# Kernel tuning notes

Measured on AMD Instinct MI355X. Metric: run time of the kernel, lower is better.

The kernel has to match this reference:

```python
import jax, jax.numpy as jnp
import numpy as np

N = 100000   # users
E = 50000    # hyperedges per timestep
NNZ = 800000 # incidences per timestep
T = 8        # step_split
D = 64       # embed_dim


def setup_inputs() -> dict:
    key = jax.random.key(0)
    ks = jax.random.split(key, 9)
    s = 1.0 / np.sqrt(D)
    return {
        "user_emb": jax.random.normal(ks[0], (N, D), jnp.float32) * s,
        "W_conv": jax.random.normal(ks[1], (D, D), jnp.float32) * s,
        "b_conv": jnp.zeros((D,), jnp.float32),
        "fus_w1": jax.random.normal(ks[2], (D, D), jnp.float32) * s,
        "fus_b1": jnp.zeros((D,), jnp.float32),
        "fus_w2": jax.random.normal(ks[3], (D, 1), jnp.float32) * s,
        "fus_b2": jnp.zeros((1,), jnp.float32),
        "edge_nodes": jax.random.randint(ks[4], (T, NNZ), 0, N),
        "edge_hyper": jax.random.randint(ks[5], (T, NNZ), 0, E),
    }


def _hconv(h, nodes, hyper):
    # h: [N, D] transformed node feats; nodes/hyper: [NNZ] incidence list
    ones = jnp.ones((nodes.shape[0], 1), h.dtype)
    e_sum = jax.ops.segment_sum(h[nodes], hyper, num_segments=E)      # [E, D]
    e_cnt = jax.ops.segment_sum(ones, hyper, num_segments=E)          # [E, 1]
    e = e_sum / jnp.maximum(e_cnt, 1.0)
    n_sum = jax.ops.segment_sum(e[hyper], nodes, num_segments=N)      # [N, D]
    n_cnt = jax.ops.segment_sum(ones, nodes, num_segments=N)          # [N, 1]
    return n_sum / jnp.maximum(n_cnt, 1.0)


def _fuse(hidden, dy, w1, b1, w2, b2):
    emb = jnp.stack([hidden, dy], axis=0)                             # [2, N, D]
    score = jax.nn.softmax(jnp.tanh(emb @ w1 + b1) @ w2 + b2, axis=0)  # [2, N, 1]
    return jnp.sum(score * emb, axis=0)                                # [N, D]


def reference(user_emb, W_conv, b_conv, fus_w1, fus_b1, fus_w2, fus_b2,
              edge_nodes, edge_hyper):
    # Conv input is always the raw user embedding table -> per-step convs independent.
    h = jax.nn.relu(user_emb @ W_conv + b_conv)                        # [N, D]
    conv_out = jax.vmap(lambda nd, hy: _hconv(h, nd, hy))(edge_nodes, edge_hyper)  # [T, N, D]

    def step(carry, dy):
        out = _fuse(carry, dy, fus_w1, fus_b1, fus_w2, fus_b2)
        return out, None

    final, _ = jax.lax.scan(step, conv_out[0], conv_out[1:])
    return final
```

## Files before the change

### kernel.cpp

```cpp
#include <hip/hip_runtime.h>
#include <hip/hip_bf16.h>

#define N_USERS 100000
#define E_HYPER 50000
#define NNZ_E   800000
#define T_STEPS 8
#define DIM     64
#define IDXM    0xFFFFF

typedef __bf16 bf16x8 __attribute__((ext_vector_type(8)));
typedef float  f32x4  __attribute__((ext_vector_type(4)));

__device__ __forceinline__ float ld_in(const void* p, size_t i, int f32)
{
    return f32 ? ((const float*)p)[i]
               : __bfloat162float(((const __hip_bfloat16*)p)[i]);
}

__global__ void k_detect(const unsigned short* __restrict__ raw, int* __restrict__ flag)
{
    __shared__ int cnt;
    if (threadIdx.x == 0) cnt = 0;
    __syncthreads();
    int c = 0;
    for (int i = threadIdx.x; i < 4096; i += blockDim.x) {
        int e = (raw[i] >> 7) & 0xFF;
        if (e > 126) c++;
    }
    atomicAdd(&cnt, c);
    __syncthreads();
    if (threadIdx.x == 0) *flag = (cnt > 64) ? 1 : 0;
}

__global__ void k_convert_params(
    const void* W, const void* b, const void* w1, const void* b1,
    const void* w2, const void* b2, const int* __restrict__ flag,
    float* __restrict__ st)
{
    int f = *flag;
    int i = blockIdx.x * blockDim.x + threadIdx.x;
    if (i < 4096)          st[i] = ld_in(W,  i,        f);
    else if (i < 4160)     st[i] = ld_in(b,  i - 4096, f);
    else if (i < 8256)     st[i] = ld_in(w1, i - 4160, f);
    else if (i < 8320)     st[i] = ld_in(b1, i - 8256, f);
    else if (i < 8384)     st[i] = ld_in(w2, i - 8320, f);
    else if (i == 8384)    st[i] = ld_in(b2, 0,        f);
}

__global__ __launch_bounds__(256) void k_transform(
    const void* __restrict__ emb, const int* __restrict__ flag,
    const float* __restrict__ st, __hip_bfloat16* __restrict__ h)
{
    __shared__ float Wl[DIM * DIM];
    __shared__ float bl[DIM];
    for (int i = threadIdx.x; i < DIM * DIM; i += blockDim.x) Wl[i] = st[i];
    if (threadIdx.x < DIM) bl[threadIdx.x] = st[4096 + threadIdx.x];
    __syncthreads();

    int f = *flag;
    int wave = threadIdx.x >> 6, lane = threadIdx.x & 63;
    int wavesTotal = gridDim.x * (blockDim.x >> 6);
    for (int row = blockIdx.x * (blockDim.x >> 6) + wave; row < N_USERS;
         row += wavesTotal) {
        size_t base = (size_t)row * DIM;
        float v = ld_in(emb, base + lane, f);
        float acc = bl[lane];
#pragma unroll
        for (int k = 0; k < DIM; ++k)
            acc += __shfl(v, k, 64) * Wl[k * DIM + lane];
        h[base + lane] = __float2bfloat16(fmaxf(acc, 0.f));
    }
}

__global__ __launch_bounds__(256) void k_build(
    const int* __restrict__ nodes, const int* __restrict__ hyper,
    int* __restrict__ head_e, int* __restrict__ next_e,
    int* __restrict__ head_n, int* __restrict__ next_n, int tag)
{
    int i = blockIdx.x * blockDim.x + threadIdx.x;
    if (i >= NNZ_E) return;
    int tv = (tag << 20) | i;
    next_e[i] = atomicExch(&head_e[hyper[i]], tv);
    next_n[i] = atomicExch(&head_n[nodes[i]], tv);
}

__device__ __forceinline__ int dec(int v, int tag)
{
    return ((v >> 20) == tag) ? (v & IDXM) : -1;
}

__global__ __launch_bounds__(256) void k_gather_e(
    const __hip_bfloat16* __restrict__ h,
    const int* __restrict__ nodes,
    const int* __restrict__ head_e, const int* __restrict__ next_e,
    __hip_bfloat16* __restrict__ e, int tag)
{
    int lane = threadIdx.x & 63;
    int wid = blockIdx.x * (blockDim.x >> 6) + (threadIdx.x >> 6);
    int nW  = gridDim.x * (blockDim.x >> 6);
    for (int s0 = wid * 8; s0 < E_HYPER; s0 += nW * 8) {
        int idx[8]; float acc[8]; int cnt[8];
#pragma unroll
        for (int c = 0; c < 8; ++c) {
            int sg = s0 + c;
            idx[c] = (sg < E_HYPER) ? dec(head_e[sg], tag) : -1;
            acc[c] = 0.f; cnt[c] = 0;
        }
        while (true) {
            bool any = false;
#pragma unroll
            for (int c = 0; c < 8; ++c) any = any || (idx[c] >= 0);
            if (!any) break;
            int nxt[8], nd[8];
#pragma unroll
            for (int c = 0; c < 8; ++c)
                if (idx[c] >= 0) { nxt[c] = next_e[idx[c]]; nd[c] = nodes[idx[c]]; }
#pragma unroll
            for (int c = 0; c < 8; ++c)
                if (idx[c] >= 0) {
                    acc[c] += __bfloat162float(h[(size_t)nd[c] * DIM + lane]);
                    cnt[c]++; idx[c] = dec(nxt[c], tag);
                }
        }
#pragma unroll
        for (int c = 0; c < 8; ++c) {
            int sg = s0 + c;
            if (sg < E_HYPER)
                e[(size_t)sg * DIM + lane] =
                    __float2bfloat16(acc[c] / (float)max(cnt[c], 1));
        }
    }
}

__device__ __forceinline__ float ld_carry(void* out, float* cws, size_t i,
                                          int f, int use_ws)
{
    if (f) return ((float*)out)[i];
    if (use_ws) return cws[i];
    return __bfloat162float(((__hip_bfloat16*)out)[i]);
}
__device__ __forceinline__ void st_carry(void* out, float* cws, size_t i,
                                         int f, int use_ws, int wr, float v)
{
    if (f) { ((float*)out)[i] = v; return; }
    if (use_ws) {
        cws[i] = v;
        if (wr) ((__hip_bfloat16*)out)[i] = __float2bfloat16(v);
        return;
    }
    ((__hip_bfloat16*)out)[i] = __float2bfloat16(v);
}

__global__ __launch_bounds__(256) void k_gather_n(
    const __hip_bfloat16* __restrict__ e,
    const int* __restrict__ hyper,
    const int* __restrict__ head_n, const int* __restrict__ next_n,
    float* __restrict__ dy,
    void* __restrict__ out, float* __restrict__ cws,
    const int* __restrict__ flag, int use_ws, int to_carry, int tag)
{
    int f = *flag;
    int lane = threadIdx.x & 63;
    int wid = blockIdx.x * (blockDim.x >> 6) + (threadIdx.x >> 6);
    int nW  = gridDim.x * (blockDim.x >> 6);
    for (int s0 = wid * 8; s0 < N_USERS; s0 += nW * 8) {
        int idx[8]; float acc[8]; int cnt[8];
#pragma unroll
        for (int c = 0; c < 8; ++c) {
            int sg = s0 + c;
            idx[c] = (sg < N_USERS) ? dec(head_n[sg], tag) : -1;
            acc[c] = 0.f; cnt[c] = 0;
        }
        while (true) {
            bool any = false;
#pragma unroll
            for (int c = 0; c < 8; ++c) any = any || (idx[c] >= 0);
            if (!any) break;
            int nxt[8], hy[8];
#pragma unroll
            for (int c = 0; c < 8; ++c)
                if (idx[c] >= 0) { nxt[c] = next_n[idx[c]]; hy[c] = hyper[idx[c]]; }
#pragma unroll
            for (int c = 0; c < 8; ++c)
                if (idx[c] >= 0) {
                    acc[c] += __bfloat162float(e[(size_t)hy[c] * DIM + lane]);
                    cnt[c]++; idx[c] = dec(nxt[c], tag);
                }
        }
#pragma unroll
        for (int c = 0; c < 8; ++c) {
            int sg = s0 + c;
            if (sg < N_USERS) {
                float v = acc[c] / (float)max(cnt[c], 1);
                size_t o = (size_t)sg * DIM + lane;
                if (to_carry) st_carry(out, cws, o, f, use_ws, 0, v);
                else          dy[o] = v;
            }
        }
    }
}

__global__ __launch_bounds__(256) void k_fuse_mfma(
    void* __restrict__ dout, float* __restrict__ cws,
    const float* __restrict__ dy_buf,
    const float* __restrict__ st, const int* __restrict__ flag,
    int use_ws, int write_out)
{
    int f = *flag;
    float* cf = f ? (float*)dout : (use_ws ? cws : (float*)0);
    __hip_bfloat16* cb = (__hip_bfloat16*)dout;

    int lane = threadIdx.x & 63;
    int quad = lane >> 4;
    int m    = lane & 15;

    bf16x8 bw[4][2];
    float b1v[4], w2v[4];
#pragma unroll
    for (int nt = 0; nt < 4; ++nt) {
#pragma unroll
        for (int kb = 0; kb < 2; ++kb)
#pragma unroll
            for (int j = 0; j < 8; ++j) {
                int k = kb * 32 + quad * 8 + j;
                bw[nt][kb][j] = (__bf16)st[4160 + k * 64 + nt * 16 + m];
            }
        b1v[nt] = st[8256 + nt * 16 + m];
        w2v[nt] = st[8320 + nt * 16 + m];
    }

    int wid = blockIdx.x * (blockDim.x >> 6) + (threadIdx.x >> 6);
    int nW  = gridDim.x * (blockDim.x >> 6);
    const int NT = N_USERS / 16;

    for (int tile = wid; tile < NT; tile += nW) {
        int row = tile * 16 + m;
        size_t base = (size_t)row * DIM;

        float hidf[2][8], dyf[2][8];
        if (cf) {
            const f32x4* cp = (const f32x4*)(cf + base);
            const f32x4* dp = (const f32x4*)(dy_buf + base);
#pragma unroll
            for (int kb = 0; kb < 2; ++kb) {
                f32x4 a = cp[kb * 8 + quad * 2], b = cp[kb * 8 + quad * 2 + 1];
                f32x4 c = dp[kb * 8 + quad * 2], d = dp[kb * 8 + quad * 2 + 1];
#pragma unroll
                for (int j = 0; j < 4; ++j) {
                    hidf[kb][j] = a[j]; hidf[kb][4 + j] = b[j];
                    dyf[kb][j]  = c[j]; dyf[kb][4 + j]  = d[j];
                }
            }
        } else {
#pragma unroll
            for (int kb = 0; kb < 2; ++kb)
#pragma unroll
                for (int j = 0; j < 8; ++j) {
                    int k = kb * 32 + quad * 8 + j;
                    hidf[kb][j] = __bfloat162float(cb[base + k]);
                    dyf[kb][j]  = dy_buf[base + k];
                }
        }

        bf16x8 ah[2], ad[2];
#pragma unroll
        for (int kb = 0; kb < 2; ++kb)
#pragma unroll
            for (int j = 0; j < 8; ++j) {
                ah[kb][j] = (__bf16)hidf[kb][j];
                ad[kb][j] = (__bf16)dyf[kb][j];
            }

        float zh[4] = {0.f, 0.f, 0.f, 0.f};
        float zd[4] = {0.f, 0.f, 0.f, 0.f};
#pragma unroll
        for (int nt = 0; nt < 4; ++nt) {
            f32x4 acch = {0.f, 0.f, 0.f, 0.f};
            f32x4 accd = {0.f, 0.f, 0.f, 0.f};
#pragma unroll
            for (int kb = 0; kb < 2; ++kb) {
                acch = __builtin_amdgcn_mfma_f32_16x16x32_bf16(ah[kb], bw[nt][kb], acch, 0, 0, 0);
                accd = __builtin_amdgcn_mfma_f32_16x16x32_bf16(ad[kb], bw[nt][kb], accd, 0, 0, 0);
            }
#pragma unroll
            for (int reg = 0; reg < 4; ++reg) {
                zh[reg] += tanhf(acch[reg] + b1v[nt]) * w2v[nt];
                zd[reg] += tanhf(accd[reg] + b1v[nt]) * w2v[nt];
            }
        }
        float s[4];
#pragma unroll
        for (int reg = 0; reg < 4; ++reg) {
#pragma unroll
            for (int off = 1; off < 16; off <<= 1) {
                zh[reg] += __shfl_xor(zh[reg], off, 64);
                zd[reg] += __shfl_xor(zd[reg], off, 64);
            }
            float mm = fmaxf(zh[reg], zd[reg]);
            float eh = expf(zh[reg] - mm), ed = expf(zd[reg] - mm);
            s[reg] = eh / (eh + ed);
        }
        int srcl = (m >> 2) * 16;
        float s0 = __shfl(s[0], srcl, 64), s1 = __shfl(s[1], srcl, 64);
        float s2 = __shfl(s[2], srcl, 64), s3 = __shfl(s[3], srcl, 64);
        int r3 = m & 3;
        float sv = (r3 == 0) ? s0 : (r3 == 1) ? s1 : (r3 == 2) ? s2 : s3;

        if (cf) {
            f32x4* cp = (f32x4*)(cf + base);
#pragma unroll
            for (int kb = 0; kb < 2; ++kb) {
                f32x4 v0, v1;
#pragma unroll
                for (int j = 0; j < 4; ++j) {
                    v0[j] = sv * hidf[kb][j]     + (1.f - sv) * dyf[kb][j];
                    v1[j] = sv * hidf[kb][4 + j] + (1.f - sv) * dyf[kb][4 + j];
                }
                cp[kb * 8 + quad * 2]     = v0;
                cp[kb * 8 + quad * 2 + 1] = v1;
                if (write_out && !f) {
#pragma unroll
                    for (int j = 0; j < 4; ++j) {
                        int k = kb * 32 + quad * 8 + j;
                        cb[base + k]     = __float2bfloat16(v0[j]);
                        cb[base + k + 4] = __float2bfloat16(v1[j]);
                    }
                }
            }
        } else {
#pragma unroll
            for (int kb = 0; kb < 2; ++kb)
#pragma unroll
                for (int j = 0; j < 8; ++j) {
                    int k = kb * 32 + quad * 8 + j;
                    float v = sv * hidf[kb][j] + (1.f - sv) * dyf[kb][j];
                    cb[base + k] = __float2bfloat16(v);
                }
        }
    }
}

extern "C" void kernel_launch(void* const* d_in, const int* in_sizes, int n_in,
                              void* d_out, int out_size, void* d_ws,
                              size_t ws_size, hipStream_t stream)
{
    const void* user_emb = d_in[0];
    const void* W_conv   = d_in[1];
    const void* b_conv   = d_in[2];
    const void* fus_w1   = d_in[3];
    const void* fus_b1   = d_in[4];
    const void* fus_w2   = d_in[5];
    const void* fus_b2   = d_in[6];
    const int* edge_nodes = (const int*)d_in[7];
    const int* edge_hyper = (const int*)d_in[8];

    const size_t ND = (size_t)N_USERS * DIM;

    float* ws = (float*)d_ws;
    int*   flag   = (int*)ws;
    float* st     = ws + 16;
    int*   head_e = (int*)(ws + 8464);
    int*   head_n = (int*)(ws + 58464);
    int*   next_e = (int*)(ws + 158464);
    int*   next_n = (int*)(ws + 958464);
    __hip_bfloat16* e_buf = (__hip_bfloat16*)(ws + 1758464);
    float* dy_buf = ws + 3358464;
    __hip_bfloat16* h = (__hip_bfloat16*)(ws + 9758464);
    float* carry_ws   = ws + 12958464;

    const size_t need_ws_carry = (12958464 + ND) * 4;
    const int use_ws = (ws_size >= need_ws_carry) ? 1 : 0;

    k_detect<<<1, 256, 0, stream>>>((const unsigned short*)user_emb, flag);
    k_convert_params<<<(8385 + 255) / 256, 256, 0, stream>>>(
        W_conv, b_conv, fus_w1, fus_b1, fus_w2, fus_b2, flag, st);
    k_transform<<<1024, 256, 0, stream>>>(user_emb, flag, st, h);

    for (int t = 0; t < T_STEPS; ++t) {
        const int* nodes = edge_nodes + (size_t)t * NNZ_E;
        const int* hyper = edge_hyper + (size_t)t * NNZ_E;
        int tag = t + 1;

        k_build<<<(NNZ_E + 255) / 256, 256, 0, stream>>>(
            nodes, hyper, head_e, next_e, head_n, next_n, tag);
        k_gather_e<<<1563, 256, 0, stream>>>(h, nodes, head_e, next_e, e_buf, tag);
        k_gather_n<<<3125, 256, 0, stream>>>(
            e_buf, hyper, head_n, next_n, dy_buf,
            d_out, carry_ws, flag, use_ws, (t == 0) ? 1 : 0, tag);

        if (t > 0) {
            k_fuse_mfma<<<1024, 256, 0, stream>>>(
                d_out, carry_ws, dy_buf, st, flag, use_ws,
                (t == T_STEPS - 1) ? 1 : 0);
        }
    }
}
```

Baseline: 1.996 ms.

## Overlap per-step build and fuse with gathers through horizontally merged kernels

Merges independent work into shared launches. The transform runs alongside the first list build, the fuse for step t-1 runs alongside the hyperedge gather of step t, and the list build for step t+1 runs alongside the node gather of step t. The linked-list head and next buffers are double-buffered so the next step's build cannot clobber the lists in use. The dy intermediate is also stored as bf16 instead of fp32, which halves its traffic but adds rounding error. The aim is fewer launches and better device fill; the cost is more workspace and lower precision in dy.

```diff
diff --git a/kernel.cpp b/kernel.cpp
--- a/kernel.cpp
+++ b/kernel.cpp
@@ -8,6 +8,12 @@
 #define DIM     64
 #define IDXM    0xFFFFF
 
+#define TR_BLOCKS 1024
+#define GE_BLOCKS 1563
+#define GN_BLOCKS 3125
+#define B_BLOCKS  3125
+#define FU_BLOCKS 1024
+
 typedef __bf16 bf16x8 __attribute__((ext_vector_type(8)));
 typedef float  f32x4  __attribute__((ext_vector_type(4)));
 
@@ -15,6 +21,30 @@
 {
     return f32 ? ((const float*)p)[i]
                : __bfloat162float(((const __hip_bfloat16*)p)[i]);
+}
+
+__device__ __forceinline__ int dec(int v, int tag)
+{
+    return ((v >> 20) == tag) ? (v & IDXM) : -1;
+}
+
+__device__ __forceinline__ float ld_carry(void* out, float* cws, size_t i,
+                                          int f, int use_ws)
+{
+    if (f) return ((float*)out)[i];
+    if (use_ws) return cws[i];
+    return __bfloat162float(((__hip_bfloat16*)out)[i]);
+}
+__device__ __forceinline__ void st_carry(void* out, float* cws, size_t i,
+                                         int f, int use_ws, int wr, float v)
+{
+    if (f) { ((float*)out)[i] = v; return; }
+    if (use_ws) {
+        cws[i] = v;
+        if (wr) ((__hip_bfloat16*)out)[i] = __float2bfloat16(v);
+        return;
+    }
+    ((__hip_bfloat16*)out)[i] = __float2bfloat16(v);
 }
 
 __global__ void k_detect(const unsigned short* __restrict__ raw, int* __restrict__ flag)
@@ -47,63 +77,31 @@
     else if (i == 8384)    st[i] = ld_in(b2, 0,        f);
 }
 
-__global__ __launch_bounds__(256) void k_transform(
-    const void* __restrict__ emb, const int* __restrict__ flag,
-    const float* __restrict__ st, __hip_bfloat16* __restrict__ h)
-{
-    __shared__ float Wl[DIM * DIM];
-    __shared__ float bl[DIM];
-    for (int i = threadIdx.x; i < DIM * DIM; i += blockDim.x) Wl[i] = st[i];
-    if (threadIdx.x < DIM) bl[threadIdx.x] = st[4096 + threadIdx.x];
-    __syncthreads();
-
-    int f = *flag;
-    int wave = threadIdx.x >> 6, lane = threadIdx.x & 63;
-    int wavesTotal = gridDim.x * (blockDim.x >> 6);
-    for (int row = blockIdx.x * (blockDim.x >> 6) + wave; row < N_USERS;
-         row += wavesTotal) {
-        size_t base = (size_t)row * DIM;
-        float v = ld_in(emb, base + lane, f);
-        float acc = bl[lane];
-#pragma unroll
-        for (int k = 0; k < DIM; ++k)
-            acc += __shfl(v, k, 64) * Wl[k * DIM + lane];
-        h[base + lane] = __float2bfloat16(fmaxf(acc, 0.f));
-    }
-}
-
-__global__ __launch_bounds__(256) void k_build(
+__device__ __forceinline__ void build_body(
     const int* __restrict__ nodes, const int* __restrict__ hyper,
-    int* __restrict__ head_e, int* __restrict__ next_e,
-    int* __restrict__ head_n, int* __restrict__ next_n, int tag)
-{
-    int i = blockIdx.x * blockDim.x + threadIdx.x;
+    int* __restrict__ he, int* __restrict__ ne,
+    int* __restrict__ hn, int* __restrict__ nn, int tag, int i)
+{
     if (i >= NNZ_E) return;
     int tv = (tag << 20) | i;
-    next_e[i] = atomicExch(&head_e[hyper[i]], tv);
-    next_n[i] = atomicExch(&head_n[nodes[i]], tv);
-}
-
-__device__ __forceinline__ int dec(int v, int tag)
-{
-    return ((v >> 20) == tag) ? (v & IDXM) : -1;
-}
-
-__global__ __launch_bounds__(256) void k_gather_e(
-    const __hip_bfloat16* __restrict__ h,
-    const int* __restrict__ nodes,
-    const int* __restrict__ head_e, const int* __restrict__ next_e,
-    __hip_bfloat16* __restrict__ e, int tag)
-{
-    int lane = threadIdx.x & 63;
-    int wid = blockIdx.x * (blockDim.x >> 6) + (threadIdx.x >> 6);
-    int nW  = gridDim.x * (blockDim.x >> 6);
+    ne[i] = atomicExch(&he[hyper[i]], tv);
+    nn[i] = atomicExch(&hn[nodes[i]], tv);
+}
+
+__device__ __forceinline__ void ge_body(
+    const __hip_bfloat16* __restrict__ h, const int* __restrict__ nodes,
+    const int* __restrict__ he, const int* __restrict__ ne,
+    __hip_bfloat16* __restrict__ e, int tag, int bid, int nblocks, int tid)
+{
+    int lane = tid & 63;
+    int wid = bid * 4 + (tid >> 6);
+    int nW  = nblocks * 4;
     for (int s0 = wid * 8; s0 < E_HYPER; s0 += nW * 8) {
         int idx[8]; float acc[8]; int cnt[8];
 #pragma unroll
         for (int c = 0; c < 8; ++c) {
             int sg = s0 + c;
-            idx[c] = (sg < E_HYPER) ? dec(head_e[sg], tag) : -1;
+            idx[c] = (sg < E_HYPER) ? dec(he[sg], tag) : -1;
             acc[c] = 0.f; cnt[c] = 0;
         }
         while (true) {
@@ -114,7 +112,7 @@
             int nxt[8], nd[8];
 #pragma unroll
             for (int c = 0; c < 8; ++c)
-                if (idx[c] >= 0) { nxt[c] = next_e[idx[c]]; nd[c] = nodes[idx[c]]; }
+                if (idx[c] >= 0) { nxt[c] = ne[idx[c]]; nd[c] = nodes[idx[c]]; }
 #pragma unroll
             for (int c = 0; c < 8; ++c)
                 if (idx[c] >= 0) {
@@ -132,43 +130,22 @@
     }
 }
 
-__device__ __forceinline__ float ld_carry(void* out, float* cws, size_t i,
-                                          int f, int use_ws)
-{
-    if (f) return ((float*)out)[i];
-    if (use_ws) return cws[i];
-    return __bfloat162float(((__hip_bfloat16*)out)[i]);
-}
-__device__ __forceinline__ void st_carry(void* out, float* cws, size_t i,
-                                         int f, int use_ws, int wr, float v)
-{
-    if (f) { ((float*)out)[i] = v; return; }
-    if (use_ws) {
-        cws[i] = v;
-        if (wr) ((__hip_bfloat16*)out)[i] = __float2bfloat16(v);
-        return;
-    }
-    ((__hip_bfloat16*)out)[i] = __float2bfloat16(v);
-}
-
-__global__ __launch_bounds__(256) void k_gather_n(
-    const __hip_bfloat16* __restrict__ e,
-    const int* __restrict__ hyper,
-    const int* __restrict__ head_n, const int* __restrict__ next_n,
-    float* __restrict__ dy,
-    void* __restrict__ out, float* __restrict__ cws,
-    const int* __restrict__ flag, int use_ws, int to_carry, int tag)
-{
-    int f = *flag;
-    int lane = threadIdx.x & 63;
-    int wid = blockIdx.x * (blockDim.x >> 6) + (threadIdx.x >> 6);
-    int nW  = gridDim.x * (blockDim.x >> 6);
+__device__ __forceinline__ void gn_body(
+    const __hip_bfloat16* __restrict__ e, const int* __restrict__ hyper,
+    const int* __restrict__ hn, const int* __restrict__ nn,
+    __hip_bfloat16* __restrict__ dyb, void* __restrict__ dout,
+    float* __restrict__ cws, int f, int use_ws, int to_carry, int tag,
+    int bid, int nblocks, int tid)
+{
+    int lane = tid & 63;
+    int wid = bid * 4 + (tid >> 6);
+    int nW  = nblocks * 4;
     for (int s0 = wid * 8; s0 < N_USERS; s0 += nW * 8) {
         int idx[8]; float acc[8]; int cnt[8];
 #pragma unroll
         for (int c = 0; c < 8; ++c) {
             int sg = s0 + c;
-            idx[c] = (sg < N_USERS) ? dec(head_n[sg], tag) : -1;
+            idx[c] = (sg < N_USERS) ? dec(hn[sg], tag) : -1;
             acc[c] = 0.f; cnt[c] = 0;
         }
         while (true) {
@@ -179,7 +156,7 @@
             int nxt[8], hy[8];
 #pragma unroll
             for (int c = 0; c < 8; ++c)
-                if (idx[c] >= 0) { nxt[c] = next_n[idx[c]]; hy[c] = hyper[idx[c]]; }
+                if (idx[c] >= 0) { nxt[c] = nn[idx[c]]; hy[c] = hyper[idx[c]]; }
 #pragma unroll
             for (int c = 0; c < 8; ++c)
                 if (idx[c] >= 0) {
@@ -193,24 +170,22 @@
             if (sg < N_USERS) {
                 float v = acc[c] / (float)max(cnt[c], 1);
                 size_t o = (size_t)sg * DIM + lane;
-                if (to_carry) st_carry(out, cws, o, f, use_ws, 0, v);
-                else          dy[o] = v;
-            }
-        }
-    }
-}
-
-__global__ __launch_bounds__(256) void k_fuse_mfma(
+                if (to_carry) st_carry(dout, cws, o, f, use_ws, 0, v);
+                else          dyb[o] = __float2bfloat16(v);
+            }
+        }
+    }
+}
+
+__device__ __forceinline__ void fu_body(
     void* __restrict__ dout, float* __restrict__ cws,
-    const float* __restrict__ dy_buf,
-    const float* __restrict__ st, const int* __restrict__ flag,
-    int use_ws, int write_out)
-{
-    int f = *flag;
+    const __hip_bfloat16* __restrict__ dyb, const float* __restrict__ st,
+    int f, int use_ws, int write_out, int bid, int nblocks, int tid)
+{
     float* cf = f ? (float*)dout : (use_ws ? cws : (float*)0);
     __hip_bfloat16* cb = (__hip_bfloat16*)dout;
 
-    int lane = threadIdx.x & 63;
+    int lane = tid & 63;
     int quad = lane >> 4;
     int m    = lane & 15;
 
@@ -229,8 +204,8 @@
         w2v[nt] = st[8320 + nt * 16 + m];
     }
 
-    int wid = blockIdx.x * (blockDim.x >> 6) + (threadIdx.x >> 6);
-    int nW  = gridDim.x * (blockDim.x >> 6);
+    int wid = bid * 4 + (tid >> 6);
+    int nW  = nblocks * 4;
     const int NT = N_USERS / 16;
 
     for (int tile = wid; tile < NT; tile += nW) {
@@ -238,38 +213,28 @@
         size_t base = (size_t)row * DIM;
 
         float hidf[2][8], dyf[2][8];
-        if (cf) {
-            const f32x4* cp = (const f32x4*)(cf + base);
-            const f32x4* dp = (const f32x4*)(dy_buf + base);
-#pragma unroll
-            for (int kb = 0; kb < 2; ++kb) {
+        bf16x8 ah[2], ad[2];
+#pragma unroll
+        for (int kb = 0; kb < 2; ++kb) {
+            ad[kb] = *(const bf16x8*)(const void*)(dyb + base + kb * 32 + quad * 8);
+#pragma unroll
+            for (int j = 0; j < 8; ++j) dyf[kb][j] = (float)ad[kb][j];
+            if (cf) {
+                const f32x4* cp = (const f32x4*)(cf + base);
                 f32x4 a = cp[kb * 8 + quad * 2], b = cp[kb * 8 + quad * 2 + 1];
-                f32x4 c = dp[kb * 8 + quad * 2], d = dp[kb * 8 + quad * 2 + 1];
 #pragma unroll
                 for (int j = 0; j < 4; ++j) {
                     hidf[kb][j] = a[j]; hidf[kb][4 + j] = b[j];
-                    dyf[kb][j]  = c[j]; dyf[kb][4 + j]  = d[j];
-                }
-            }
-        } else {
-#pragma unroll
-            for (int kb = 0; kb < 2; ++kb)
-#pragma unroll
-                for (int j = 0; j < 8; ++j) {
-                    int k = kb * 32 + quad * 8 + j;
-                    hidf[kb][j] = __bfloat162float(cb[base + k]);
-                    dyf[kb][j]  = dy_buf[base + k];
-                }
-        }
-
-        bf16x8 ah[2], ad[2];
-#pragma unroll
-        for (int kb = 0; kb < 2; ++kb)
-#pragma unroll
-            for (int j = 0; j < 8; ++j) {
-                ah[kb][j] = (__bf16)hidf[kb][j];
-                ad[kb][j] = (__bf16)dyf[kb][j];
-            }
+                }
+#pragma unroll
+                for (int j = 0; j < 8; ++j) ah[kb][j] = (__bf16)hidf[kb][j];
+            } else {
+                bf16x8 hv = *(const bf16x8*)(const void*)(cb + base + kb * 32 + quad * 8);
+                ah[kb] = hv;
+#pragma unroll
+                for (int j = 0; j < 8; ++j) hidf[kb][j] = (float)hv[j];
+            }
+        }
 
         float zh[4] = {0.f, 0.f, 0.f, 0.f};
         float zd[4] = {0.f, 0.f, 0.f, 0.f};
@@ -337,6 +302,72 @@
                     cb[base + k] = __float2bfloat16(v);
                 }
         }
+    }
+}
+
+__global__ __launch_bounds__(256) void k_trans_build(
+    const void* __restrict__ emb, const int* __restrict__ flag,
+    const float* __restrict__ st, __hip_bfloat16* __restrict__ h,
+    const int* __restrict__ nodes, const int* __restrict__ hyper,
+    int* __restrict__ he, int* __restrict__ ne,
+    int* __restrict__ hn, int* __restrict__ nn, int tag)
+{
+    __shared__ float Wl[DIM * DIM];
+    __shared__ float bl[DIM];
+    if ((int)blockIdx.x < TR_BLOCKS) {
+        for (int i = threadIdx.x; i < DIM * DIM; i += blockDim.x) Wl[i] = st[i];
+        if (threadIdx.x < DIM) bl[threadIdx.x] = st[4096 + threadIdx.x];
+        __syncthreads();
+        int f = *flag;
+        int wave = threadIdx.x >> 6, lane = threadIdx.x & 63;
+        int nW = TR_BLOCKS * 4;
+        for (int row = blockIdx.x * 4 + wave; row < N_USERS; row += nW) {
+            size_t base = (size_t)row * DIM;
+            float v = ld_in(emb, base + lane, f);
+            float acc = bl[lane];
+#pragma unroll
+            for (int k = 0; k < DIM; ++k)
+                acc += __shfl(v, k, 64) * Wl[k * DIM + lane];
+            h[base + lane] = __float2bfloat16(fmaxf(acc, 0.f));
+        }
+    } else {
+        int i = (blockIdx.x - TR_BLOCKS) * blockDim.x + threadIdx.x;
+        build_body(nodes, hyper, he, ne, hn, nn, tag, i);
+    }
+}
+
+__global__ __launch_bounds__(256) void k_ge_fuse(
+    const __hip_bfloat16* __restrict__ h, const int* __restrict__ nodes,
+    const int* __restrict__ he, const int* __restrict__ ne,
+    __hip_bfloat16* __restrict__ e, int tag, int ge_blocks,
+    void* __restrict__ dout, float* __restrict__ cws,
+    const __hip_bfloat16* __restrict__ dyb, const float* __restrict__ st,
+    const int* __restrict__ flag, int use_ws, int do_fuse, int write_out)
+{
+    if ((int)blockIdx.x < ge_blocks) {
+        ge_body(h, nodes, he, ne, e, tag, blockIdx.x, ge_blocks, threadIdx.x);
+    } else if (do_fuse) {
+        fu_body(dout, cws, dyb, st, *flag, use_ws, write_out,
+                blockIdx.x - ge_blocks, gridDim.x - ge_blocks, threadIdx.x);
+    }
+}
+
+__global__ __launch_bounds__(256) void k_gn_build(
+    const __hip_bfloat16* __restrict__ e, const int* __restrict__ hyper,
+    const int* __restrict__ hn, const int* __restrict__ nn,
+    __hip_bfloat16* __restrict__ dyb, void* __restrict__ dout,
+    float* __restrict__ cws, const int* __restrict__ flag,
+    int use_ws, int to_carry, int tag, int gn_blocks,
+    const int* __restrict__ nodes1, const int* __restrict__ hyper1,
+    int* __restrict__ he1, int* __restrict__ ne1,
+    int* __restrict__ hn1, int* __restrict__ nn1, int tag1, int do_build)
+{
+    if ((int)blockIdx.x < gn_blocks) {
+        gn_body(e, hyper, hn, nn, dyb, dout, cws, *flag, use_ws, to_carry,
+                tag, blockIdx.x, gn_blocks, threadIdx.x);
+    } else if (do_build) {
+        int i = (blockIdx.x - gn_blocks) * blockDim.x + threadIdx.x;
+        build_body(nodes1, hyper1, he1, ne1, hn1, nn1, tag1, i);
     }
 }
 
@@ -357,41 +388,51 @@
     const size_t ND = (size_t)N_USERS * DIM;
 
     float* ws = (float*)d_ws;
-    int*   flag   = (int*)ws;
-    float* st     = ws + 16;
-    int*   head_e = (int*)(ws + 8464);
-    int*   head_n = (int*)(ws + 58464);
-    int*   next_e = (int*)(ws + 158464);
-    int*   next_n = (int*)(ws + 958464);
-    __hip_bfloat16* e_buf = (__hip_bfloat16*)(ws + 1758464);
-    float* dy_buf = ws + 3358464;
-    __hip_bfloat16* h = (__hip_bfloat16*)(ws + 9758464);
-    float* carry_ws   = ws + 12958464;
-
-    const size_t need_ws_carry = (12958464 + ND) * 4;
+    int*   flag = (int*)ws;
+    float* st   = ws + 16;
+    int* he[2] = {(int*)(ws + 8464),    (int*)(ws + 58464)};
+    int* hn[2] = {(int*)(ws + 108464),  (int*)(ws + 208464)};
+    int* ne[2] = {(int*)(ws + 308464),  (int*)(ws + 1108464)};
+    int* nn[2] = {(int*)(ws + 1908464), (int*)(ws + 2708464)};
+    __hip_bfloat16* e_buf = (__hip_bfloat16*)(ws + 3508464);
+    __hip_bfloat16* dyb   = (__hip_bfloat16*)(ws + 5108464);
+    __hip_bfloat16* h     = (__hip_bfloat16*)(ws + 8308464);
+    float* carry_ws       = ws + 11508464;
+
+    const size_t need_ws_carry = (11508464 + ND) * 4;
     const int use_ws = (ws_size >= need_ws_carry) ? 1 : 0;
 
     k_detect<<<1, 256, 0, stream>>>((const unsigned short*)user_emb, flag);
     k_convert_params<<<(8385 + 255) / 256, 256, 0, stream>>>(
         W_conv, b_conv, fus_w1, fus_b1, fus_w2, fus_b2, flag, st);
-    k_transform<<<1024, 256, 0, stream>>>(user_emb, flag, st, h);
+
+    k_trans_build<<<TR_BLOCKS + B_BLOCKS, 256, 0, stream>>>(
+        user_emb, flag, st, h, edge_nodes, edge_hyper,
+        he[0], ne[0], hn[0], nn[0], 1);
 
     for (int t = 0; t < T_STEPS; ++t) {
-        const int* nodes = edge_nodes + (size_t)t * NNZ_E;
-        const int* hyper = edge_hyper + (size_t)t * NNZ_E;
-        int tag = t + 1;
-
-        k_build<<<(NNZ_E + 255) / 256, 256, 0, stream>>>(
-            nodes, hyper, head_e, next_e, head_n, next_n, tag);
-        k_gather_e<<<1563, 256, 0, stream>>>(h, nodes, head_e, next_e, e_buf, tag);
-        k_gather_n<<<3125, 256, 0, stream>>>(
-            e_buf, hyper, head_n, next_n, dy_buf,
-            d_out, carry_ws, flag, use_ws, (t == 0) ? 1 : 0, tag);
-
-        if (t > 0) {
-            k_fuse_mfma<<<1024, 256, 0, stream>>>(
-                d_out, carry_ws, dy_buf, st, flag, use_ws,
-                (t == T_STEPS - 1) ? 1 : 0);
-        }
-    }
-}
+        int b  = t & 1;
+        int nb = b ^ 1;
+        const int* nodes  = edge_nodes + (size_t)t * NNZ_E;
+        const int* hyper  = edge_hyper + (size_t)t * NNZ_E;
+        const int* nodes1 = edge_nodes + (size_t)(t + 1) * NNZ_E;
+        const int* hyper1 = edge_hyper + (size_t)(t + 1) * NNZ_E;
+
+        int gridA = GE_BLOCKS + ((t > 0) ? FU_BLOCKS : 0);
+        k_ge_fuse<<<gridA, 256, 0, stream>>>(
+            h, nodes, he[b], ne[b], e_buf, t + 1, GE_BLOCKS,
+            d_out, carry_ws, dyb, st, flag, use_ws, (t > 0) ? 1 : 0, 0);
+
+        int do_b = (t < T_STEPS - 1) ? 1 : 0;
+        int gridB = GN_BLOCKS + (do_b ? B_BLOCKS : 0);
+        k_gn_build<<<gridB, 256, 0, stream>>>(
+            e_buf, hyper, hn[b], nn[b], dyb, d_out, carry_ws, flag,
+            use_ws, (t == 0) ? 1 : 0, t + 1, GN_BLOCKS,
+            do_b ? nodes1 : nodes, do_b ? hyper1 : hyper,
+            he[nb], ne[nb], hn[nb], nn[nb], t + 2, do_b);
+    }
+
+    k_ge_fuse<<<FU_BLOCKS, 256, 0, stream>>>(
+        h, edge_nodes, he[1], ne[1], e_buf, 8, 0,
+        d_out, carry_ws, dyb, st, flag, use_ws, 1, 1);
+}
```

Measured after the change: 2.685 ms. 34.5% more time.

## Co-schedule next-step list build with current fuse and transform in merged kernels

Applied to the files above, without the earlier changes.

Fuses independent work horizontally by splitting the grid's blocks between two roles. The linked-list build for step t+1 now runs in the same launch as the fusion MLP for step t, and the first build shares a launch with the dense transform. This removes one launch per timestep and lets the atomic-heavy build overlap with the bandwidth- and MFMA-bound fuse work. The tag scheme means the head arrays never need clearing. The cost is sharing one block size and register budget between both roles, which can limit occupancy for the lighter role.

```diff
diff --git a/kernel.cpp b/kernel.cpp
--- a/kernel.cpp
+++ b/kernel.cpp
@@ -8,6 +8,12 @@
 #define DIM     64
 #define IDXM    0xFFFFF
 
+#define TR_BLOCKS 1024
+#define GE_BLOCKS 1563
+#define GN_BLOCKS 3125
+#define B_BLOCKS  3125
+#define FU_BLOCKS 1024
+
 typedef __bf16 bf16x8 __attribute__((ext_vector_type(8)));
 typedef float  f32x4  __attribute__((ext_vector_type(4)));
 
@@ -15,6 +21,30 @@
 {
     return f32 ? ((const float*)p)[i]
                : __bfloat162float(((const __hip_bfloat16*)p)[i]);
+}
+
+__device__ __forceinline__ int dec(int v, int tag)
+{
+    return ((v >> 20) == tag) ? (v & IDXM) : -1;
+}
+
+__device__ __forceinline__ float ld_carry(void* out, float* cws, size_t i,
+                                          int f, int use_ws)
+{
+    if (f) return ((float*)out)[i];
+    if (use_ws) return cws[i];
+    return __bfloat162float(((__hip_bfloat16*)out)[i]);
+}
+__device__ __forceinline__ void st_carry(void* out, float* cws, size_t i,
+                                         int f, int use_ws, int wr, float v)
+{
+    if (f) { ((float*)out)[i] = v; return; }
+    if (use_ws) {
+        cws[i] = v;
+        if (wr) ((__hip_bfloat16*)out)[i] = __float2bfloat16(v);
+        return;
+    }
+    ((__hip_bfloat16*)out)[i] = __float2bfloat16(v);
 }
 
 __global__ void k_detect(const unsigned short* __restrict__ raw, int* __restrict__ flag)
@@ -47,52 +77,190 @@
     else if (i == 8384)    st[i] = ld_in(b2, 0,        f);
 }
 
-__global__ __launch_bounds__(256) void k_transform(
+__device__ __forceinline__ void build_body(
+    const int* __restrict__ nodes, const int* __restrict__ hyper,
+    int* __restrict__ he, int* __restrict__ ne,
+    int* __restrict__ hn, int* __restrict__ nn, int tag, int i)
+{
+    if (i >= NNZ_E) return;
+    int tv = (tag << 20) | i;
+    ne[i] = atomicExch(&he[hyper[i]], tv);
+    nn[i] = atomicExch(&hn[nodes[i]], tv);
+}
+
+__device__ __forceinline__ void fu_body(
+    void* __restrict__ dout, float* __restrict__ cws,
+    const float* __restrict__ dy_buf, const float* __restrict__ st,
+    int f, int use_ws, int write_out, int bid, int nblocks, int tid)
+{
+    float* cf = f ? (float*)dout : (use_ws ? cws : (float*)0);
+    __hip_bfloat16* cb = (__hip_bfloat16*)dout;
+
+    int lane = tid & 63;
+    int quad = lane >> 4;
+    int m    = lane & 15;
+
+    bf16x8 bw[4][2];
+    float b1v[4], w2v[4];
+#pragma unroll
+    for (int nt = 0; nt < 4; ++nt) {
+#pragma unroll
+        for (int kb = 0; kb < 2; ++kb)
+#pragma unroll
+            for (int j = 0; j < 8; ++j) {
+                int k = kb * 32 + quad * 8 + j;
+                bw[nt][kb][j] = (__bf16)st[4160 + k * 64 + nt * 16 + m];
+            }
+        b1v[nt] = st[8256 + nt * 16 + m];
+        w2v[nt] = st[8320 + nt * 16 + m];
+    }
+
+    int wid = bid * 4 + (tid >> 6);
+    int nW  = nblocks * 4;
+    const int NT = N_USERS / 16;
+
+    for (int tile = wid; tile < NT; tile += nW) {
+        int row = tile * 16 + m;
+        size_t base = (size_t)row * DIM;
+
+        float hidf[2][8], dyf[2][8];
+        if (cf) {
+            const f32x4* cp = (const f32x4*)(cf + base);
+            const f32x4* dp = (const f32x4*)(dy_buf + base);
+#pragma unroll
+            for (int kb = 0; kb < 2; ++kb) {
+                f32x4 a = cp[kb * 8 + quad * 2], b = cp[kb * 8 + quad * 2 + 1];
+                f32x4 c = dp[kb * 8 + quad * 2], d = dp[kb * 8 + quad * 2 + 1];
+#pragma unroll
+                for (int j = 0; j < 4; ++j) {
+                    hidf[kb][j] = a[j]; hidf[kb][4 + j] = b[j];
+                    dyf[kb][j]  = c[j]; dyf[kb][4 + j]  = d[j];
+                }
+            }
+        } else {
+#pragma unroll
+            for (int kb = 0; kb < 2; ++kb)
+#pragma unroll
+                for (int j = 0; j < 8; ++j) {
+                    int k = kb * 32 + quad * 8 + j;
+                    hidf[kb][j] = __bfloat162float(cb[base + k]);
+                    dyf[kb][j]  = dy_buf[base + k];
+                }
+        }
+
+        bf16x8 ah[2], ad[2];
+#pragma unroll
+        for (int kb = 0; kb < 2; ++kb)
+#pragma unroll
+            for (int j = 0; j < 8; ++j) {
+                ah[kb][j] = (__bf16)hidf[kb][j];
+                ad[kb][j] = (__bf16)dyf[kb][j];
+            }
+
+        float zh[4] = {0.f, 0.f, 0.f, 0.f};
+        float zd[4] = {0.f, 0.f, 0.f, 0.f};
+#pragma unroll
+        for (int nt = 0; nt < 4; ++nt) {
+            f32x4 acch = {0.f, 0.f, 0.f, 0.f};
+            f32x4 accd = {0.f, 0.f, 0.f, 0.f};
+#pragma unroll
+            for (int kb = 0; kb < 2; ++kb) {
+                acch = __builtin_amdgcn_mfma_f32_16x16x32_bf16(ah[kb], bw[nt][kb], acch, 0, 0, 0);
+                accd = __builtin_amdgcn_mfma_f32_16x16x32_bf16(ad[kb], bw[nt][kb], accd, 0, 0, 0);
+            }
+#pragma unroll
+            for (int reg = 0; reg < 4; ++reg) {
+                zh[reg] += tanhf(acch[reg] + b1v[nt]) * w2v[nt];
+                zd[reg] += tanhf(accd[reg] + b1v[nt]) * w2v[nt];
+            }
+        }
+        float s[4];
+#pragma unroll
+        for (int reg = 0; reg < 4; ++reg) {
+#pragma unroll
+            for (int off = 1; off < 16; off <<= 1) {
+                zh[reg] += __shfl_xor(zh[reg], off, 64);
+                zd[reg] += __shfl_xor(zd[reg], off, 64);
+            }
+            float mm = fmaxf(zh[reg], zd[reg]);
+            float eh = expf(zh[reg] - mm), ed = expf(zd[reg] - mm);
+            s[reg] = eh / (eh + ed);
+        }
+        int srcl = (m >> 2) * 16;
+        float s0 = __shfl(s[0], srcl, 64), s1 = __shfl(s[1], srcl, 64);
+        float s2 = __shfl(s[2], srcl, 64), s3 = __shfl(s[3], srcl, 64);
+        int r3 = m & 3;
+        float sv = (r3 == 0) ? s0 : (r3 == 1) ? s1 : (r3 == 2) ? s2 : s3;
+
+        if (cf) {
+            f32x4* cp = (f32x4*)(cf + base);
+#pragma unroll
+            for (int kb = 0; kb < 2; ++kb) {
+                f32x4 v0, v1;
+#pragma unroll
+                for (int j = 0; j < 4; ++j) {
+                    v0[j] = sv * hidf[kb][j]     + (1.f - sv) * dyf[kb][j];
+                    v1[j] = sv * hidf[kb][4 + j] + (1.f - sv) * dyf[kb][4 + j];
+                }
+                cp[kb * 8 + quad * 2]     = v0;
+                cp[kb * 8 + quad * 2 + 1] = v1;
+                if (write_out && !f) {
+#pragma unroll
+                    for (int j = 0; j < 4; ++j) {
+                        int k = kb * 32 + quad * 8 + j;
+                        cb[base + k]     = __float2bfloat16(v0[j]);
+                        cb[base + k + 4] = __float2bfloat16(v1[j]);
+                    }
+                }
+            }
+        } else {
+#pragma unroll
+            for (int kb = 0; kb < 2; ++kb)
+#pragma unroll
+                for (int j = 0; j < 8; ++j) {
+                    int k = kb * 32 + quad * 8 + j;
+                    float v = sv * hidf[kb][j] + (1.f - sv) * dyf[kb][j];
+                    cb[base + k] = __float2bfloat16(v);
+                }
+        }
+    }
+}
+
+__global__ __launch_bounds__(256) void k_trans_build(
     const void* __restrict__ emb, const int* __restrict__ flag,
-    const float* __restrict__ st, __hip_bfloat16* __restrict__ h)
+    const float* __restrict__ st, __hip_bfloat16* __restrict__ h,
+    const int* __restrict__ nodes, const int* __restrict__ hyper,
+    int* __restrict__ he, int* __restrict__ ne,
+    int* __restrict__ hn, int* __restrict__ nn, int tag)
 {
     __shared__ float Wl[DIM * DIM];
     __shared__ float bl[DIM];
-    for (int i = threadIdx.x; i < DIM * DIM; i += blockDim.x) Wl[i] = st[i];
-    if (threadIdx.x < DIM) bl[threadIdx.x] = st[4096 + threadIdx.x];
-    __syncthreads();
-
-    int f = *flag;
-    int wave = threadIdx.x >> 6, lane = threadIdx.x & 63;
-    int wavesTotal = gridDim.x * (blockDim.x >> 6);
-    for (int row = blockIdx.x * (blockDim.x >> 6) + wave; row < N_USERS;
-         row += wavesTotal) {
-        size_t base = (size_t)row * DIM;
-        float v = ld_in(emb, base + lane, f);
-        float acc = bl[lane];
-#pragma unroll
-        for (int k = 0; k < DIM; ++k)
-            acc += __shfl(v, k, 64) * Wl[k * DIM + lane];
-        h[base + lane] = __float2bfloat16(fmaxf(acc, 0.f));
-    }
-}
-
-__global__ __launch_bounds__(256) void k_build(
-    const int* __restrict__ nodes, const int* __restrict__ hyper,
-    int* __restrict__ head_e, int* __restrict__ next_e,
-    int* __restrict__ head_n, int* __restrict__ next_n, int tag)
-{
-    int i = blockIdx.x * blockDim.x + threadIdx.x;
-    if (i >= NNZ_E) return;
-    int tv = (tag << 20) | i;
-    next_e[i] = atomicExch(&head_e[hyper[i]], tv);
-    next_n[i] = atomicExch(&head_n[nodes[i]], tv);
-}
-
-__device__ __forceinline__ int dec(int v, int tag)
-{
-    return ((v >> 20) == tag) ? (v & IDXM) : -1;
+    if ((int)blockIdx.x < TR_BLOCKS) {
+        for (int i = threadIdx.x; i < DIM * DIM; i += blockDim.x) Wl[i] = st[i];
+        if (threadIdx.x < DIM) bl[threadIdx.x] = st[4096 + threadIdx.x];
+        __syncthreads();
+        int f = *flag;
+        int wave = threadIdx.x >> 6, lane = threadIdx.x & 63;
+        int nW = TR_BLOCKS * 4;
+        for (int row = blockIdx.x * 4 + wave; row < N_USERS; row += nW) {
+            size_t base = (size_t)row * DIM;
+            float v = ld_in(emb, base + lane, f);
+            float acc = bl[lane];
+#pragma unroll
+            for (int k = 0; k < DIM; ++k)
+                acc += __shfl(v, k, 64) * Wl[k * DIM + lane];
+            h[base + lane] = __float2bfloat16(fmaxf(acc, 0.f));
+        }
+    } else {
+        int i = (blockIdx.x - TR_BLOCKS) * blockDim.x + threadIdx.x;
+        build_body(nodes, hyper, he, ne, hn, nn, tag, i);
+    }
 }
 
 __global__ __launch_bounds__(256) void k_gather_e(
     const __hip_bfloat16* __restrict__ h,
     const int* __restrict__ nodes,
-    const int* __restrict__ head_e, const int* __restrict__ next_e,
+    const int* __restrict__ he, const int* __restrict__ ne,
     __hip_bfloat16* __restrict__ e, int tag)
 {
     int lane = threadIdx.x & 63;
@@ -103,7 +271,7 @@
 #pragma unroll
         for (int c = 0; c < 8; ++c) {
             int sg = s0 + c;
-            idx[c] = (sg < E_HYPER) ? dec(head_e[sg], tag) : -1;
+            idx[c] = (sg < E_HYPER) ? dec(he[sg], tag) : -1;
             acc[c] = 0.f; cnt[c] = 0;
         }
         while (true) {
@@ -114,7 +282,7 @@
             int nxt[8], nd[8];
 #pragma unroll
             for (int c = 0; c < 8; ++c)
-                if (idx[c] >= 0) { nxt[c] = next_e[idx[c]]; nd[c] = nodes[idx[c]]; }
+                if (idx[c] >= 0) { nxt[c] = ne[idx[c]]; nd[c] = nodes[idx[c]]; }
 #pragma unroll
             for (int c = 0; c < 8; ++c)
                 if (idx[c] >= 0) {
@@ -132,29 +300,10 @@
     }
 }
 
-__device__ __forceinline__ float ld_carry(void* out, float* cws, size_t i,
-                                          int f, int use_ws)
-{
-    if (f) return ((float*)out)[i];
-    if (use_ws) return cws[i];
-    return __bfloat162float(((__hip_bfloat16*)out)[i]);
-}
-__device__ __forceinline__ void st_carry(void* out, float* cws, size_t i,
-                                         int f, int use_ws, int wr, float v)
-{
-    if (f) { ((float*)out)[i] = v; return; }
-    if (use_ws) {
-        cws[i] = v;
-        if (wr) ((__hip_bfloat16*)out)[i] = __float2bfloat16(v);
-        return;
-    }
-    ((__hip_bfloat16*)out)[i] = __float2bfloat16(v);
-}
-
 __global__ __launch_bounds__(256) void k_gather_n(
     const __hip_bfloat16* __restrict__ e,
     const int* __restrict__ hyper,
-    const int* __restrict__ head_n, const int* __restrict__ next_n,
+    const int* __restrict__ hn, const int* __restrict__ nn,
     float* __restrict__ dy,
     void* __restrict__ out, float* __restrict__ cws,
     const int* __restrict__ flag, int use_ws, int to_carry, int tag)
@@ -168,7 +317,7 @@
 #pragma unroll
         for (int c = 0; c < 8; ++c) {
             int sg = s0 + c;
-            idx[c] = (sg < N_USERS) ? dec(head_n[sg], tag) : -1;
+            idx[c] = (sg < N_USERS) ? dec(hn[sg], tag) : -1;
             acc[c] = 0.f; cnt[c] = 0;
         }
         while (true) {
@@ -179,7 +328,7 @@
             int nxt[8], hy[8];
 #pragma unroll
             for (int c = 0; c < 8; ++c)
-                if (idx[c] >= 0) { nxt[c] = next_n[idx[c]]; hy[c] = hyper[idx[c]]; }
+                if (idx[c] >= 0) { nxt[c] = nn[idx[c]]; hy[c] = hyper[idx[c]]; }
 #pragma unroll
             for (int c = 0; c < 8; ++c)
                 if (idx[c] >= 0) {
@@ -200,143 +349,20 @@
     }
 }
 
-__global__ __launch_bounds__(256) void k_fuse_mfma(
+__global__ __launch_bounds__(256) void k_build_fuse(
+    const int* __restrict__ nodes1, const int* __restrict__ hyper1,
+    int* __restrict__ he, int* __restrict__ ne,
+    int* __restrict__ hn, int* __restrict__ nn, int tag1, int nbuild,
     void* __restrict__ dout, float* __restrict__ cws,
-    const float* __restrict__ dy_buf,
-    const float* __restrict__ st, const int* __restrict__ flag,
-    int use_ws, int write_out)
-{
-    int f = *flag;
-    float* cf = f ? (float*)dout : (use_ws ? cws : (float*)0);
-    __hip_bfloat16* cb = (__hip_bfloat16*)dout;
-
-    int lane = threadIdx.x & 63;
-    int quad = lane >> 4;
-    int m    = lane & 15;
-
-    bf16x8 bw[4][2];
-    float b1v[4], w2v[4];
-#pragma unroll
-    for (int nt = 0; nt < 4; ++nt) {
-#pragma unroll
-        for (int kb = 0; kb < 2; ++kb)
-#pragma unroll
-            for (int j = 0; j < 8; ++j) {
-                int k = kb * 32 + quad * 8 + j;
-                bw[nt][kb][j] = (__bf16)st[4160 + k * 64 + nt * 16 + m];
-            }
-        b1v[nt] = st[8256 + nt * 16 + m];
-        w2v[nt] = st[8320 + nt * 16 + m];
-    }
-
-    int wid = blockIdx.x * (blockDim.x >> 6) + (threadIdx.x >> 6);
-    int nW  = gridDim.x * (blockDim.x >> 6);
-    const int NT = N_USERS / 16;
-
-    for (int tile = wid; tile < NT; tile += nW) {
-        int row = tile * 16 + m;
-        size_t base = (size_t)row * DIM;
-
-        float hidf[2][8], dyf[2][8];
-        if (cf) {
-            const f32x4* cp = (const f32x4*)(cf + base);
-            const f32x4* dp = (const f32x4*)(dy_buf + base);
-#pragma unroll
-            for (int kb = 0; kb < 2; ++kb) {
-                f32x4 a = cp[kb * 8 + quad * 2], b = cp[kb * 8 + quad * 2 + 1];
-                f32x4 c = dp[kb * 8 + quad * 2], d = dp[kb * 8 + quad * 2 + 1];
-#pragma unroll
-                for (int j = 0; j < 4; ++j) {
-                    hidf[kb][j] = a[j]; hidf[kb][4 + j] = b[j];
-                    dyf[kb][j]  = c[j]; dyf[kb][4 + j]  = d[j];
-                }
-            }
-        } else {
-#pragma unroll
-            for (int kb = 0; kb < 2; ++kb)
-#pragma unroll
-                for (int j = 0; j < 8; ++j) {
-                    int k = kb * 32 + quad * 8 + j;
-                    hidf[kb][j] = __bfloat162float(cb[base + k]);
-                    dyf[kb][j]  = dy_buf[base + k];
-                }
-        }
-
-        bf16x8 ah[2], ad[2];
-#pragma unroll
-        for (int kb = 0; kb < 2; ++kb)
-#pragma unroll
-            for (int j = 0; j < 8; ++j) {
-                ah[kb][j] = (__bf16)hidf[kb][j];
-                ad[kb][j] = (__bf16)dyf[kb][j];
-            }
-
-        float zh[4] = {0.f, 0.f, 0.f, 0.f};
-        float zd[4] = {0.f, 0.f, 0.f, 0.f};
-#pragma unroll
-        for (int nt = 0; nt < 4; ++nt) {
-            f32x4 acch = {0.f, 0.f, 0.f, 0.f};
-            f32x4 accd = {0.f, 0.f, 0.f, 0.f};
-#pragma unroll
-            for (int kb = 0; kb < 2; ++kb) {
-                acch = __builtin_amdgcn_mfma_f32_16x16x32_bf16(ah[kb], bw[nt][kb], acch, 0, 0, 0);
-                accd = __builtin_amdgcn_mfma_f32_16x16x32_bf16(ad[kb], bw[nt][kb], accd, 0, 0, 0);
-            }
-#pragma unroll
-            for (int reg = 0; reg < 4; ++reg) {
-                zh[reg] += tanhf(acch[reg] + b1v[nt]) * w2v[nt];
-                zd[reg] += tanhf(accd[reg] + b1v[nt]) * w2v[nt];
-            }
-        }
-        float s[4];
-#pragma unroll
-        for (int reg = 0; reg < 4; ++reg) {
-#pragma unroll
-            for (int off = 1; off < 16; off <<= 1) {
-                zh[reg] += __shfl_xor(zh[reg], off, 64);
-                zd[reg] += __shfl_xor(zd[reg], off, 64);
-            }
-            float mm = fmaxf(zh[reg], zd[reg]);
-            float eh = expf(zh[reg] - mm), ed = expf(zd[reg] - mm);
-            s[reg] = eh / (eh + ed);
-        }
-        int srcl = (m >> 2) * 16;
-        float s0 = __shfl(s[0], srcl, 64), s1 = __shfl(s[1], srcl, 64);
-        float s2 = __shfl(s[2], srcl, 64), s3 = __shfl(s[3], srcl, 64);
-        int r3 = m & 3;
-        float sv = (r3 == 0) ? s0 : (r3 == 1) ? s1 : (r3 == 2) ? s2 : s3;
-
-        if (cf) {
-            f32x4* cp = (f32x4*)(cf + base);
-#pragma unroll
-            for (int kb = 0; kb < 2; ++kb) {
-                f32x4 v0, v1;
-#pragma unroll
-                for (int j = 0; j < 4; ++j) {
-                    v0[j] = sv * hidf[kb][j]     + (1.f - sv) * dyf[kb][j];
-                    v1[j] = sv * hidf[kb][4 + j] + (1.f - sv) * dyf[kb][4 + j];
-                }
-                cp[kb * 8 + quad * 2]     = v0;
-                cp[kb * 8 + quad * 2 + 1] = v1;
-                if (write_out && !f) {
-#pragma unroll
-                    for (int j = 0; j < 4; ++j) {
-                        int k = kb * 32 + quad * 8 + j;
-                        cb[base + k]     = __float2bfloat16(v0[j]);
-                        cb[base + k + 4] = __float2bfloat16(v1[j]);
-                    }
-                }
-            }
-        } else {
-#pragma unroll
-            for (int kb = 0; kb < 2; ++kb)
-#pragma unroll
-                for (int j = 0; j < 8; ++j) {
-                    int k = kb * 32 + quad * 8 + j;
-                    float v = sv * hidf[kb][j] + (1.f - sv) * dyf[kb][j];
-                    cb[base + k] = __float2bfloat16(v);
-                }
-        }
+    const float* __restrict__ dy_buf, const float* __restrict__ st,
+    const int* __restrict__ flag, int use_ws, int do_fuse, int write_out)
+{
+    if ((int)blockIdx.x < nbuild) {
+        int i = blockIdx.x * blockDim.x + threadIdx.x;
+        build_body(nodes1, hyper1, he, ne, hn, nn, tag1, i);
+    } else if (do_fuse) {
+        fu_body(dout, cws, dy_buf, st, *flag, use_ws, write_out,
+                blockIdx.x - nbuild, gridDim.x - nbuild, threadIdx.x);
     }
 }
 
@@ -374,24 +400,32 @@
     k_detect<<<1, 256, 0, stream>>>((const unsigned short*)user_emb, flag);
     k_convert_params<<<(8385 + 255) / 256, 256, 0, stream>>>(
         W_conv, b_conv, fus_w1, fus_b1, fus_w2, fus_b2, flag, st);
-    k_transform<<<1024, 256, 0, stream>>>(user_emb, flag, st, h);
+
+    k_trans_build<<<TR_BLOCKS + B_BLOCKS, 256, 0, stream>>>(
+        user_emb, flag, st, h, edge_nodes, edge_hyper,
+        head_e, next_e, head_n, next_n, 1);
 
     for (int t = 0; t < T_STEPS; ++t) {
-        const int* nodes = edge_nodes + (size_t)t * NNZ_E;
-        const int* hyper = edge_hyper + (size_t)t * NNZ_E;
+        const int* nodes  = edge_nodes + (size_t)t * NNZ_E;
+        const int* hyper  = edge_hyper + (size_t)t * NNZ_E;
+        const int* nodes1 = edge_nodes + (size_t)(t + 1) * NNZ_E;
+        const int* hyper1 = edge_hyper + (size_t)(t + 1) * NNZ_E;
         int tag = t + 1;
 
-        k_build<<<(NNZ_E + 255) / 256, 256, 0, stream>>>(
-            nodes, hyper, head_e, next_e, head_n, next_n, tag);
-        k_gather_e<<<1563, 256, 0, stream>>>(h, nodes, head_e, next_e, e_buf, tag);
-        k_gather_n<<<3125, 256, 0, stream>>>(
+        k_gather_e<<<GE_BLOCKS, 256, 0, stream>>>(
+            h, nodes, head_e, next_e, e_buf, tag);
+        k_gather_n<<<GN_BLOCKS, 256, 0, stream>>>(
             e_buf, hyper, head_n, next_n, dy_buf,
             d_out, carry_ws, flag, use_ws, (t == 0) ? 1 : 0, tag);
 
-        if (t > 0) {
-            k_fuse_mfma<<<1024, 256, 0, stream>>>(
-                d_out, carry_ws, dy_buf, st, flag, use_ws,
-                (t == T_STEPS - 1) ? 1 : 0);
-        }
-    }
-}
+        int do_b  = (t < T_STEPS - 1) ? 1 : 0;
+        int do_f  = (t > 0) ? 1 : 0;
+        int nb    = do_b ? B_BLOCKS : 0;
+        int grid  = nb + (do_f ? FU_BLOCKS : 0);
+        k_build_fuse<<<grid, 256, 0, stream>>>(
+            do_b ? nodes1 : nodes, do_b ? hyper1 : hyper,
+            head_e, next_e, head_n, next_n, t + 2, nb,
+            d_out, carry_ws, dy_buf, st, flag, use_ws, do_f,
+            (t == T_STEPS - 1) ? 1 : 0);
+    }
+}
```

New measurement: 1.976 ms. No clear change (-1.0%).
